# Kernel optimization log

Hardware: AMD Instinct MI355X
Metric: run time of the kernel (lower is better)

## Reference

```python
import jax, jax.numpy as jnp
import numpy as np

# Static configuration (matches init_kwargs / input_specs)
F, K = 64, 3            # filters, kernel_size
B, H, W, C = 64, 32, 32, 8
S = 1                   # strides (VALID padding, stride 1)
O1, O2 = H - K + 1, W - K + 1
L = O1 * O2             # output_lenght
N = H * W               # Right_shape[0]*Right_shape[1] (VALID -> no pad)
NTRI = K * ((K - 1) // 2) * K // K * 1  # per-filter strict-triangular count
NTRI = K * (K - 1) // 2  # = k*floor((k-1)/2) for odd k (3 for k=3)


def _phi_n_indices():
    """Column indices of the sparse phi operator, per set_indices_phi.
    For VALID/stride-1 the window start for output i=(r,c) is r*W + c.
    Returns int array (L, K*K) with n = block*W + start + j."""
    r = np.arange(O1)
    c = np.arange(O2)
    start = (r[:, None] * W + c[None, :]).reshape(L)          # (L,)
    blk = np.arange(K)[:, None] * W + np.arange(K)[None, :]   # (K,K)
    n = start[:, None, None] + blk[None]                      # (L,K,K)
    return n.reshape(L, K * K)

_N_IDX = jnp.asarray(_phi_n_indices())          # (L, K*K) static
_TI, _TJ = np.triu_indices(K, 1)                # strict upper, row-major
_LI, _LJ = np.tril_indices(K, -1)               # strict lower, row-major


def setup_inputs() -> dict:
    key = jax.random.key(0)
    ks = jax.random.split(key, 6)
    u = lambda k_, shp: jax.random.uniform(k_, shp, jnp.float32, -0.05, 0.05)
    return {
        "inputs": jax.random.normal(ks[0], (B, H, W, C), jnp.float32),
        "omega_diag": u(ks[1], (F, K)),
        "omega_triu": u(ks[2], (1, F * NTRI)),
        "omega_tril": u(ks[3], (1, F * NTRI)),
        "lambda_in": u(ks[4], (K, 1)),
        "lambda_out": u(ks[5], (1, K)),
        "use_encode": jnp.ones((1, N), jnp.float32),
        "use_decode": jnp.zeros((L, 1), jnp.float32),
    }


def reference(inputs, omega_diag, omega_triu, omega_tril,
              lambda_in, lambda_out, use_encode, use_decode):
    # flatten + matrix_pad (identity for VALID) + channel mean
    up = inputs.reshape(B, N, C).mean(axis=-1)                # (B, N)

    # Assemble omega = tril + diag + triu, per filter (F,K,K)
    omega = jnp.zeros((F, K, K), inputs.dtype)
    omega = omega.at[:, _TI, _TJ].set(omega_triu.reshape(F, NTRI))
    omega = omega.at[:, _LI, _LJ].set(omega_tril.reshape(F, NTRI))
    omega = omega.at[:, jnp.arange(K), jnp.arange(K)].set(omega_diag)
    base = omega * (lambda_in - lambda_out)                   # (F,K,K)

    # Scatter base into the dense phi operator (F, L, N)
    vals = jnp.broadcast_to(base.reshape(F, 1, K * K), (F, L, K * K))
    kernel = jnp.zeros((F, L, N), inputs.dtype)
    kernel = kernel.at[:, jnp.arange(L)[:, None], _N_IDX].set(vals)

    # kernel @ diag(encode) - diag(decode) @ kernel  (column/row scaling)
    kernel = kernel * use_encode[0][None, None, :] \
             - use_decode[:, 0][None, :, None] * kernel

    # (F,L,N) x (B,N) -> (B,L,F), then to image layout
    out = jnp.einsum('fln,bn->blf', kernel, up)
    out = out.reshape(B, O1, O2, F)
    return jax.nn.relu(out)
```

## Files before the change

kernel.cpp:

```cpp
#include <hip/hip_runtime.h>


#define SPL 16

__global__ __launch_bounds__(256) void spectral_conv_kernel(
    const float* __restrict__ inputs,
    const float* __restrict__ om_diag,
    const float* __restrict__ om_triu,
    const float* __restrict__ om_tril,
    const float* __restrict__ lam_in,
    const float* __restrict__ lam_out,
    const float* __restrict__ enc,
    const float* __restrict__ dec,
    float* __restrict__ out)
{
    __shared__ float up_s[1024];
    __shared__ float ue_s[1024];

    const int tid   = threadIdx.x;
    const int b     = (int)blockIdx.x & 63;
    const int split = (int)blockIdx.x >> 6;

    const float* img = inputs + (size_t)b * 8192;
    #pragma unroll
    for (int k = 0; k < 4; ++k) {
        int m = tid + 256 * k;
        const float4* p4 = (const float4*)(img + m * 8);
        float4 a = p4[0];
        float4 q = p4[1];
        float u = (a.x + a.y + a.z + a.w + q.x + q.y + q.z + q.w) * 0.125f;
        up_s[m] = u;
        ue_s[m] = u * enc[m];
    }
    __syncthreads();

    const int f   = tid & 63;
    const int wid = tid >> 6;
    const float li0 = lam_in[0],  li1 = lam_in[1],  li2 = lam_in[2];
    const float lo0 = lam_out[0], lo1 = lam_out[1], lo2 = lam_out[2];
    const float w00 = om_diag[f * 3 + 0] * (li0 - lo0);
    const float w01 = om_triu[f * 3 + 0] * (li0 - lo1);
    const float w02 = om_triu[f * 3 + 1] * (li0 - lo2);
    const float w10 = om_tril[f * 3 + 0] * (li1 - lo0);
    const float w11 = om_diag[f * 3 + 1] * (li1 - lo1);
    const float w12 = om_triu[f * 3 + 2] * (li1 - lo2);
    const float w20 = om_tril[f * 3 + 1] * (li2 - lo0);
    const float w21 = om_tril[f * 3 + 2] * (li2 - lo1);
    const float w22 = om_diag[f * 3 + 2] * (li2 - lo2);

    float* outb = out + (size_t)b * (900 * 64);

    for (int p = split * 4 + wid; p < 900; p += 4 * SPL) {
        const int r  = p / 30;
        const int c  = p - r * 30;
        const int n0 = r * 32 + c;
        const float dl = dec[p];

        float s1, s2;
        s1 = w00 * ue_s[n0 +  0];            s2 = w00 * up_s[n0 +  0];
        s1 = fmaf(w01, ue_s[n0 +  1], s1);   s2 = fmaf(w01, up_s[n0 +  1], s2);
        s1 = fmaf(w02, ue_s[n0 +  2], s1);   s2 = fmaf(w02, up_s[n0 +  2], s2);
        s1 = fmaf(w10, ue_s[n0 + 32], s1);   s2 = fmaf(w10, up_s[n0 + 32], s2);
        s1 = fmaf(w11, ue_s[n0 + 33], s1);   s2 = fmaf(w11, up_s[n0 + 33], s2);
        s1 = fmaf(w12, ue_s[n0 + 34], s1);   s2 = fmaf(w12, up_s[n0 + 34], s2);
        s1 = fmaf(w20, ue_s[n0 + 64], s1);   s2 = fmaf(w20, up_s[n0 + 64], s2);
        s1 = fmaf(w21, ue_s[n0 + 65], s1);   s2 = fmaf(w21, up_s[n0 + 65], s2);
        s1 = fmaf(w22, ue_s[n0 + 66], s1);   s2 = fmaf(w22, up_s[n0 + 66], s2);

        outb[p * 64 + f] = fmaxf(fmaf(-dl, s2, s1), 0.0f);
    }
}

extern "C" void kernel_launch(void* const* d_in, const int* in_sizes, int n_in,
                              void* d_out, int out_size, void* d_ws, size_t ws_size,
                              hipStream_t stream) {
    const float* inputs  = (const float*)d_in[0];
    const float* om_diag = (const float*)d_in[1];
    const float* om_triu = (const float*)d_in[2];
    const float* om_tril = (const float*)d_in[3];
    const float* lam_in  = (const float*)d_in[4];
    const float* lam_out = (const float*)d_in[5];
    const float* enc     = (const float*)d_in[6];
    const float* dec     = (const float*)d_in[7];
    float* out = (float*)d_out;

    dim3 grid(64 * SPL);
    dim3 block(256);
    spectral_conv_kernel<<<grid, block, 0, stream>>>(
        inputs, om_diag, om_triu, om_tril, lam_in, lam_out, enc, dec, out);
}
```

Before: 79.12 us.

## Tile outputs as 2x4 register patches per wavefront with vectorized LDS loads

Each wavefront now computes a 2-row by 4-column patch of output pixels. It first loads a 4x8 window of the pooled and encoded images from shared memory into registers with float4 reads, then reuses those registers across neighbouring stencil taps. The grid grows from 16 to 30 splits per image so that 120 wavefronts cover the 15x8 patch grid. This removes per-pixel division, scalar LDS reads and loop overhead, at the cost of more registers and slightly padded shared arrays for the edge reads.

```diff
diff --git a/kernel.cpp b/kernel.cpp
--- a/kernel.cpp
+++ b/kernel.cpp
@@ -1,7 +1,7 @@
 #include <hip/hip_runtime.h>
 
 
-#define SPL 16
+#define SPL 30
 
 __global__ __launch_bounds__(256) void spectral_conv_kernel(
     const float* __restrict__ inputs,
@@ -14,8 +14,10 @@
     const float* __restrict__ dec,
     float* __restrict__ out)
 {
-    __shared__ float up_s[1024];
-    __shared__ float ue_s[1024];
+    __shared__ float4 up4[257];
+    __shared__ float4 ue4[257];
+    float* up_s = (float*)up4;
+    float* ue_s = (float*)ue4;
 
     const int tid   = threadIdx.x;
     const int b     = (int)blockIdx.x & 63;
@@ -48,26 +50,52 @@
     const float w21 = om_tril[f * 3 + 2] * (li2 - lo1);
     const float w22 = om_diag[f * 3 + 2] * (li2 - lo2);
 
+    const int sg = split * 4 + wid;
+    const int r0 = (sg >> 3) * 2;
+    const int cb = (sg & 7) * 4;
+
+    float Ur[4][8], Er[4][8];
+    #pragma unroll
+    for (int rw = 0; rw < 4; ++rw) {
+        int b4 = (((r0 + rw) << 5) + cb) >> 2;
+        *(float4*)&Ur[rw][0] = up4[b4];
+        *(float4*)&Ur[rw][4] = up4[b4 + 1];
+        *(float4*)&Er[rw][0] = ue4[b4];
+        *(float4*)&Er[rw][4] = ue4[b4 + 1];
+    }
+
+    const int p0 = r0 * 30 + cb;
     float* outb = out + (size_t)b * (900 * 64);
 
-    for (int p = split * 4 + wid; p < 900; p += 4 * SPL) {
-        const int r  = p / 30;
-        const int c  = p - r * 30;
-        const int n0 = r * 32 + c;
-        const float dl = dec[p];
+    #pragma unroll
+    for (int q = 0; q < 4; ++q) {
+        if (cb + q < 30) {
+            float s1 = w00 * Er[0][q];
+            float s2 = w00 * Ur[0][q];
+            s1 = fmaf(w01, Er[0][q+1], s1);  s2 = fmaf(w01, Ur[0][q+1], s2);
+            s1 = fmaf(w02, Er[0][q+2], s1);  s2 = fmaf(w02, Ur[0][q+2], s2);
+            s1 = fmaf(w10, Er[1][q  ], s1);  s2 = fmaf(w10, Ur[1][q  ], s2);
+            s1 = fmaf(w11, Er[1][q+1], s1);  s2 = fmaf(w11, Ur[1][q+1], s2);
+            s1 = fmaf(w12, Er[1][q+2], s1);  s2 = fmaf(w12, Ur[1][q+2], s2);
+            s1 = fmaf(w20, Er[2][q  ], s1);  s2 = fmaf(w20, Ur[2][q  ], s2);
+            s1 = fmaf(w21, Er[2][q+1], s1);  s2 = fmaf(w21, Ur[2][q+1], s2);
+            s1 = fmaf(w22, Er[2][q+2], s1);  s2 = fmaf(w22, Ur[2][q+2], s2);
+            float dl0 = dec[p0 + q];
+            outb[(p0 + q) * 64 + f] = fmaxf(fmaf(-dl0, s2, s1), 0.0f);
 
-        float s1, s2;
-        s1 = w00 * ue_s[n0 +  0];            s2 = w00 * up_s[n0 +  0];
-        s1 = fmaf(w01, ue_s[n0 +  1], s1);   s2 = fmaf(w01, up_s[n0 +  1], s2);
-        s1 = fmaf(w02, ue_s[n0 +  2], s1);   s2 = fmaf(w02, up_s[n0 +  2], s2);
-        s1 = fmaf(w10, ue_s[n0 + 32], s1);   s2 = fmaf(w10, up_s[n0 + 32], s2);
-        s1 = fmaf(w11, ue_s[n0 + 33], s1);   s2 = fmaf(w11, up_s[n0 + 33], s2);
-        s1 = fmaf(w12, ue_s[n0 + 34], s1);   s2 = fmaf(w12, up_s[n0 + 34], s2);
-        s1 = fmaf(w20, ue_s[n0 + 64], s1);   s2 = fmaf(w20, up_s[n0 + 64], s2);
-        s1 = fmaf(w21, ue_s[n0 + 65], s1);   s2 = fmaf(w21, up_s[n0 + 65], s2);
-        s1 = fmaf(w22, ue_s[n0 + 66], s1);   s2 = fmaf(w22, up_s[n0 + 66], s2);
-
-        outb[p * 64 + f] = fmaxf(fmaf(-dl, s2, s1), 0.0f);
+            float t1 = w00 * Er[1][q];
+            float t2 = w00 * Ur[1][q];
+            t1 = fmaf(w01, Er[1][q+1], t1);  t2 = fmaf(w01, Ur[1][q+1], t2);
+            t1 = fmaf(w02, Er[1][q+2], t1);  t2 = fmaf(w02, Ur[1][q+2], t2);
+            t1 = fmaf(w10, Er[2][q  ], t1);  t2 = fmaf(w10, Ur[2][q  ], t2);
+            t1 = fmaf(w11, Er[2][q+1], t1);  t2 = fmaf(w11, Ur[2][q+1], t2);
+            t1 = fmaf(w12, Er[2][q+2], t1);  t2 = fmaf(w12, Ur[2][q+2], t2);
+            t1 = fmaf(w20, Er[3][q  ], t1);  t2 = fmaf(w20, Ur[3][q  ], t2);
+            t1 = fmaf(w21, Er[3][q+1], t1);  t2 = fmaf(w21, Ur[3][q+1], t2);
+            t1 = fmaf(w22, Er[3][q+2], t1);  t2 = fmaf(w22, Ur[3][q+2], t2);
+            float dl1 = dec[p0 + 30 + q];
+            outb[(p0 + 30 + q) * 64 + f] = fmaxf(fmaf(-dl1, t2, t1), 0.0f);
+        }
     }
 }
 
```

New measurement: 78.29 us. Within noise of the previous version (-1.0%).
